# Optimization experiments

Hardware: AMD Instinct MI355X
Metric: run time of the kernel (lower is better)

## Reference

```python
import jax, jax.numpy as jnp
import numpy as np

N = 50000      # nodes
E = 640000     # edges (before self loops)
IN = 128       # in_channels
H = 4          # heads (layer 1)
C = 64         # hidden_channels per head
OUT = 64       # out_channels
SLOPE = 0.2    # PyG GATConv default negative_slope


def setup_inputs() -> dict:
    key = jax.random.key(0)
    ks = jax.random.split(key, 12)
    x = jax.random.normal(ks[0], (N, IN), dtype=jnp.float32)
    edge_src = jax.random.randint(ks[1], (E,), 0, N, dtype=jnp.int32)
    edge_dst = jax.random.randint(ks[2], (E,), 0, N, dtype=jnp.int32)
    # Layer 1 params: Linear IN -> H*C, attention vectors a_src/a_dst [H, C], bias [H*C]
    W1 = jax.random.normal(ks[3], (IN, H * C), dtype=jnp.float32) / np.sqrt(IN)
    att_src1 = jax.random.normal(ks[4], (H, C), dtype=jnp.float32) / np.sqrt(C)
    att_dst1 = jax.random.normal(ks[5], (H, C), dtype=jnp.float32) / np.sqrt(C)
    b1 = jnp.zeros((H * C,), dtype=jnp.float32)
    # Layer 2 params: Linear H*C -> OUT, 1 head
    W2 = jax.random.normal(ks[6], (H * C, OUT), dtype=jnp.float32) / np.sqrt(H * C)
    att_src2 = jax.random.normal(ks[7], (1, OUT), dtype=jnp.float32) / np.sqrt(OUT)
    att_dst2 = jax.random.normal(ks[8], (1, OUT), dtype=jnp.float32) / np.sqrt(OUT)
    b2 = jnp.zeros((OUT,), dtype=jnp.float32)
    return {"x": x, "W1": W1, "att_src1": att_src1, "att_dst1": att_dst1, "b1": b1,
            "W2": W2, "att_src2": att_src2, "att_dst2": att_dst2, "b2": b2,
            "edge_src": edge_src, "edge_dst": edge_dst}


def gat_conv(x, src, dst, W, a_src, a_dst, b, heads, ch):
    """PyG GATConv (concat=True): gather -> LeakyReLU attention -> per-dst softmax -> scatter-add."""
    n = x.shape[0]
    h = (x @ W).reshape(n, heads, ch)                  # [N, H, C]
    al_s = jnp.sum(h * a_src, axis=-1)                 # [N, H] node-level src attention term
    al_d = jnp.sum(h * a_dst, axis=-1)                 # [N, H]
    e = jax.nn.leaky_relu(al_s[src] + al_d[dst], SLOPE)  # [E, H] edge scores
    m = jax.ops.segment_max(e, dst, num_segments=n)    # stable per-dst softmax
    ex = jnp.exp(e - m[dst])
    den = jax.ops.segment_sum(ex, dst, num_segments=n)
    alpha = ex / den[dst]                              # [E, H]
    msg = h[src] * alpha[:, :, None]                   # [E, H, C]
    out = jax.ops.segment_sum(msg, dst, num_segments=n)  # [N, H, C]
    return out.reshape(n, heads * ch) + b


def reference(x, W1, att_src1, att_dst1, b1, W2, att_src2, att_dst2, b2, edge_src, edge_dst):
    # PyG GATConv default add_self_loops=True
    loops = jnp.arange(N, dtype=edge_src.dtype)
    src = jnp.concatenate([edge_src, loops])
    dst = jnp.concatenate([edge_dst, loops])
    h = gat_conv(x, src, dst, W1, att_src1, att_dst1, b1, H, C)
    h = jax.nn.elu(h)                                  # F.elu; dropout p=0 -> no-op
    out = gat_conv(h, src, dst, W2, att_src2, att_dst2, b2, 1, OUT)
    return out
```

## Files before the change

### kernel.cpp

```cpp
#include <hip/hip_runtime.h>
#include <hip/hip_bf16.h>
#include <cstdint>
#include <cstddef>

#define N_NODES 50000
#define N_EDGES 640000
#define ET (N_EDGES + N_NODES)
#define IN_CH 128
#define H1 4
#define HC1 256
#define OUT_CH 64
#define SLOPE 0.2f
#define SCAN_NBLK ((N_NODES + 255) / 256)
#define XW (N_NODES * IN_CH / 8)
#define W1N (IN_CH * HC1)
#define W2N (HC1 * OUT_CH)
#define CONVB ((XW + W1N + W2N + 255) / 256)
#define EDGEB ((ET + 255) / 256)
#define MT ((N_NODES + 63) / 64)
#define G1B (4 * MT)

typedef __attribute__((ext_vector_type(8))) short short8;
typedef __attribute__((ext_vector_type(4))) float floatx4;

__device__ __forceinline__ float bf2f(unsigned short u) {
    return __uint_as_float(((unsigned)u) << 16);
}
__device__ __forceinline__ unsigned short f2bf(float f) {
    unsigned u = __float_as_uint(f);
    unsigned r = 0x7fffu + ((u >> 16) & 1u);
    return (unsigned short)((u + r) >> 16);
}
__device__ __forceinline__ float ldf(const void* p, size_t i, bool f32) {
    return f32 ? ((const float*)p)[i] : bf2f(((const unsigned short*)p)[i]);
}

__global__ __launch_bounds__(256) void init_all(
    const unsigned short* __restrict__ x, unsigned* __restrict__ flag,
    int* __restrict__ counts, int* __restrict__ state)
{
    int b = blockIdx.x;
    if (b < SCAN_NBLK) {
        int i = b * 256 + threadIdx.x;
        if (i < N_NODES) counts[i] = 0;
    } else {
        int t = threadIdx.x;
        if (t < 64) {
            int bad = 0;
            #pragma unroll
            for (int r = 0; r < 4; ++r) {
                float v = bf2f(x[r * 64 + t]);
                if (!(v == v) || fabsf(v) > 1e4f) bad = 1;
            }
            unsigned long long m = __ballot(bad != 0);
            if (t == 0) *flag = (m != 0ull) ? 1u : 0u;
        } else if (t == 64) {
            state[0] = 0; state[1] = 0;
        }
    }
}

__global__ __launch_bounds__(256) void conv_count(
    const void* __restrict__ x, const void* __restrict__ W1,
    const void* __restrict__ W2, const unsigned* __restrict__ flag,
    unsigned short* __restrict__ x16,
    unsigned short* __restrict__ Wt1, unsigned short* __restrict__ Wt2,
    const int* __restrict__ edst, int* __restrict__ counts)
{
    int b = blockIdx.x;
    if (b < CONVB) {
        int i = b * 256 + threadIdx.x;
        const bool f32 = (*flag != 0);
        if (i < XW) {
            size_t off = (size_t)i * 8;
            uint4 st;
            if (f32) {
                const float* xp = (const float*)x + off;
                float4 a = *(const float4*)xp;
                float4 c = *(const float4*)(xp + 4);
                st.x = (unsigned)f2bf(a.x) | ((unsigned)f2bf(a.y) << 16);
                st.y = (unsigned)f2bf(a.z) | ((unsigned)f2bf(a.w) << 16);
                st.z = (unsigned)f2bf(c.x) | ((unsigned)f2bf(c.y) << 16);
                st.w = (unsigned)f2bf(c.z) | ((unsigned)f2bf(c.w) << 16);
            } else {
                st = *(const uint4*)((const unsigned short*)x + off);
            }
            *(uint4*)(x16 + off) = st;
        } else if (i < XW + W1N) {
            int j = i - XW;
            int n = j / IN_CH, k = j % IN_CH;
            Wt1[j] = f2bf(ldf(W1, (size_t)k * HC1 + n, f32));
        } else if (i < XW + W1N + W2N) {
            int j = i - XW - W1N;
            int n = j / HC1, k = j % HC1;
            Wt2[j] = f2bf(ldf(W2, (size_t)k * OUT_CH + n, f32));
        }
    } else {
        int i = (b - CONVB) * 256 + threadIdx.x;
        if (i < ET) {
            int d = (i < N_EDGES) ? edst[i] : (i - N_EDGES);
            atomicAdd(&counts[d], 1);
        }
    }
}

__global__ __launch_bounds__(256) void scan_onepass(
    const int* __restrict__ counts, int* __restrict__ rowptr,
    int* __restrict__ cursor, int* __restrict__ bsum,
    int* __restrict__ boff, int* __restrict__ state)
{
    __shared__ int s[256];
    const int t = threadIdx.x, b = blockIdx.x;
    const int i = b * 256 + t;
    int v = (i < N_NODES) ? counts[i] : 0;
    s[t] = v;
    __syncthreads();
    #pragma unroll
    for (int off = 1; off < 256; off <<= 1) {
        int u = (t >= off) ? s[t - off] : 0;
        __syncthreads();
        s[t] += u;
        __syncthreads();
    }
    const int incl = s[t];
    if (t == 255) {
        __hip_atomic_store(&bsum[b], incl, __ATOMIC_RELAXED, __HIP_MEMORY_SCOPE_AGENT);
        __hip_atomic_fetch_add(&state[0], 1, __ATOMIC_ACQ_REL, __HIP_MEMORY_SCOPE_AGENT);
    }
    if (b == 0) {
        if (t == 0) {
            while (__hip_atomic_load(&state[0], __ATOMIC_ACQUIRE, __HIP_MEMORY_SCOPE_AGENT) < SCAN_NBLK)
                __builtin_amdgcn_s_sleep(8);
        }
        __syncthreads();
        int w = (t < SCAN_NBLK)
              ? __hip_atomic_load(&bsum[t], __ATOMIC_RELAXED, __HIP_MEMORY_SCOPE_AGENT) : 0;
        s[t] = w;
        __syncthreads();
        #pragma unroll
        for (int off = 1; off < 256; off <<= 1) {
            int u = (t >= off) ? s[t - off] : 0;
            __syncthreads();
            s[t] += u;
            __syncthreads();
        }
        if (t < SCAN_NBLK)
            __hip_atomic_store(&boff[t], s[t] - w, __ATOMIC_RELAXED, __HIP_MEMORY_SCOPE_AGENT);
        __syncthreads();
        if (t == 0)
            __hip_atomic_store(&state[1], 1, __ATOMIC_RELEASE, __HIP_MEMORY_SCOPE_AGENT);
    }
    if (t == 0) {
        while (__hip_atomic_load(&state[1], __ATOMIC_ACQUIRE, __HIP_MEMORY_SCOPE_AGENT) == 0)
            __builtin_amdgcn_s_sleep(8);
    }
    __syncthreads();
    int off0 = __hip_atomic_load(&boff[b], __ATOMIC_RELAXED, __HIP_MEMORY_SCOPE_AGENT);
    if (i < N_NODES) {
        int r = off0 + incl - v;
        rowptr[i] = r; cursor[i] = r;
    }
    if (i == 0) rowptr[N_NODES] = ET;
}

template <int KK>
__device__ __forceinline__ void gemm_body(
    const unsigned short* __restrict__ A, const unsigned short* __restrict__ Bt,
    const void* __restrict__ avs, const void* __restrict__ avd,
    const unsigned* __restrict__ flag, unsigned short* __restrict__ C,
    float* __restrict__ als, float* __restrict__ ald,
    int M, int N, int bx, int by)
{
    const int tid = threadIdx.x;
    const int m0 = by * 64, n0 = bx * 64;
    const int w = tid >> 6, lane = tid & 63;
    const int ln = lane & 15, quad = lane >> 4;
    const int m_frag = m0 + w * 16 + ln;
    floatx4 acc[4] = {{0.f,0.f,0.f,0.f},{0.f,0.f,0.f,0.f},{0.f,0.f,0.f,0.f},{0.f,0.f,0.f,0.f}};

    #pragma unroll
    for (int ks = 0; ks < KK / 32; ++ks) {
        const int kbase = ks * 32 + quad * 8;
        short8 a;
        if (m_frag < M) {
            a = *(const short8*)(A + (size_t)m_frag * KK + kbase);
        } else {
            #pragma unroll
            for (int j = 0; j < 8; ++j) a[j] = 0;
        }
        #pragma unroll
        for (int sub = 0; sub < 4; ++sub) {
            short8 b = *(const short8*)(Bt + (size_t)(n0 + sub * 16 + ln) * KK + kbase);
            acc[sub] = __builtin_amdgcn_mfma_f32_16x16x32_bf16(a, b, acc[sub], 0, 0, 0);
        }
    }

    #pragma unroll
    for (int sub = 0; sub < 4; ++sub) {
        #pragma unroll
        for (int r = 0; r < 4; ++r) {
            int m = m0 + w * 16 + quad * 4 + r;
            if (m < M)
                C[(size_t)m * N + n0 + sub * 16 + ln] = f2bf(acc[sub][r]);
        }
    }

    const bool f32in = (*flag != 0);
    float as[4], av[4];
    #pragma unroll
    for (int sub = 0; sub < 4; ++sub) {
        as[sub] = ldf(avs, n0 + sub * 16 + ln, f32in);
        av[sub] = ldf(avd, n0 + sub * 16 + ln, f32in);
    }
    const int Hh = N >> 6;
    #pragma unroll
    for (int r = 0; r < 4; ++r) {
        float ps = 0.f, pd = 0.f;
        #pragma unroll
        for (int sub = 0; sub < 4; ++sub) {
            ps += acc[sub][r] * as[sub];
            pd += acc[sub][r] * av[sub];
        }
        #pragma unroll
        for (int off = 1; off < 16; off <<= 1) {
            ps += __shfl_xor(ps, off, 64);
            pd += __shfl_xor(pd, off, 64);
        }
        int m = m0 + w * 16 + quad * 4 + r;
        if (ln == 0 && m < M) {
            als[(size_t)m * Hh + bx] = ps;
            ald[(size_t)m * Hh + bx] = pd;
        }
    }
}

__global__ __launch_bounds__(256) void gemm1_fill(
    const unsigned short* __restrict__ x16, const unsigned short* __restrict__ Wt1,
    const void* __restrict__ as1, const void* __restrict__ ad1,
    const unsigned* __restrict__ flag, unsigned short* __restrict__ h16,
    float* __restrict__ als, float* __restrict__ ald,
    const int* __restrict__ esrc, const int* __restrict__ edst,
    int* __restrict__ cursor, int* __restrict__ ecsr)
{
    int b = blockIdx.x;
    if (b < G1B) {
        gemm_body<IN_CH>(x16, Wt1, as1, ad1, flag, h16, als, ald,
                         N_NODES, HC1, b & 3, b >> 2);
    } else {
        int i = (b - G1B) * 256 + threadIdx.x;
        if (i < ET) {
            int s = (i < N_EDGES) ? esrc[i] : (i - N_EDGES);
            int d = (i < N_EDGES) ? edst[i] : (i - N_EDGES);
            int pos = atomicAdd(&cursor[d], 1);
            ecsr[pos] = s;
        }
    }
}

__global__ __launch_bounds__(256) void gemm2(
    const unsigned short* __restrict__ xo16, const unsigned short* __restrict__ Wt2,
    const void* __restrict__ as2, const void* __restrict__ ad2,
    const unsigned* __restrict__ flag, unsigned short* __restrict__ h2,
    float* __restrict__ als, float* __restrict__ ald)
{
    gemm_body<HC1>(xo16, Wt2, as2, ad2, flag, h2, als, ald,
                   N_NODES, OUT_CH, 0, blockIdx.x);
}

__global__ __launch_bounds__(256) void agg_node1(
    const int* __restrict__ rowptr, const int* __restrict__ ecsr,
    const unsigned short* __restrict__ h, const float* __restrict__ als,
    const float* __restrict__ ald, const void* __restrict__ bias,
    const unsigned* __restrict__ flag, unsigned short* __restrict__ out)
{
    int wave = (blockIdx.x * blockDim.x + threadIdx.x) >> 6;
    int lane = threadIdx.x & 63;
    if (wave >= N_NODES) return;
    const int d = wave;
    const int hg = lane >> 4;
    const int c0 = (lane & 15) << 2;
    const int lo = rowptr[d], hi = rowptr[d + 1];
    const float ad = ald[d * H1 + hg];

    float acc0 = 0.f, acc1 = 0.f, acc2 = 0.f, acc3 = 0.f, den = 0.f;

    int e = lo;
    for (; e + 3 < hi; e += 4) {
        int s0 = ecsr[e], s1 = ecsr[e + 1], s2 = ecsr[e + 2], s3 = ecsr[e + 3];
        uint2 q0 = *(const uint2*)(h + (size_t)s0 * HC1 + hg * 64 + c0);
        uint2 q1 = *(const uint2*)(h + (size_t)s1 * HC1 + hg * 64 + c0);
        uint2 q2 = *(const uint2*)(h + (size_t)s2 * HC1 + hg * 64 + c0);
        uint2 q3 = *(const uint2*)(h + (size_t)s3 * HC1 + hg * 64 + c0);
        float t0 = als[s0 * H1 + hg] + ad;
        float t1 = als[s1 * H1 + hg] + ad;
        float t2 = als[s2 * H1 + hg] + ad;
        float t3 = als[s3 * H1 + hg] + ad;
        t0 = (t0 > 0.f) ? t0 : SLOPE * t0;
        t1 = (t1 > 0.f) ? t1 : SLOPE * t1;
        t2 = (t2 > 0.f) ? t2 : SLOPE * t2;
        t3 = (t3 > 0.f) ? t3 : SLOPE * t3;
        float p0 = __expf(t0), p1 = __expf(t1), p2 = __expf(t2), p3 = __expf(t3);
        den += (p0 + p1) + (p2 + p3);
        acc0 += p0 * __uint_as_float(q0.x << 16)         + p1 * __uint_as_float(q1.x << 16)
              + p2 * __uint_as_float(q2.x << 16)         + p3 * __uint_as_float(q3.x << 16);
        acc1 += p0 * __uint_as_float(q0.x & 0xffff0000u) + p1 * __uint_as_float(q1.x & 0xffff0000u)
              + p2 * __uint_as_float(q2.x & 0xffff0000u) + p3 * __uint_as_float(q3.x & 0xffff0000u);
        acc2 += p0 * __uint_as_float(q0.y << 16)         + p1 * __uint_as_float(q1.y << 16)
              + p2 * __uint_as_float(q2.y << 16)         + p3 * __uint_as_float(q3.y << 16);
        acc3 += p0 * __uint_as_float(q0.y & 0xffff0000u) + p1 * __uint_as_float(q1.y & 0xffff0000u)
              + p2 * __uint_as_float(q2.y & 0xffff0000u) + p3 * __uint_as_float(q3.y & 0xffff0000u);
    }
    for (; e < hi; ++e) {
        int s0 = ecsr[e];
        uint2 q0 = *(const uint2*)(h + (size_t)s0 * HC1 + hg * 64 + c0);
        float t0 = als[s0 * H1 + hg] + ad;
        t0 = (t0 > 0.f) ? t0 : SLOPE * t0;
        float p0 = __expf(t0);
        den += p0;
        acc0 += p0 * __uint_as_float(q0.x << 16);
        acc1 += p0 * __uint_as_float(q0.x & 0xffff0000u);
        acc2 += p0 * __uint_as_float(q0.y << 16);
        acc3 += p0 * __uint_as_float(q0.y & 0xffff0000u);
    }

    const bool f32in = (*flag != 0);
    const float inv = 1.f / den;
    float v0 = acc0 * inv + ldf(bias, hg * 64 + c0 + 0, f32in);
    float v1 = acc1 * inv + ldf(bias, hg * 64 + c0 + 1, f32in);
    float v2 = acc2 * inv + ldf(bias, hg * 64 + c0 + 2, f32in);
    float v3 = acc3 * inv + ldf(bias, hg * 64 + c0 + 3, f32in);
    v0 = (v0 > 0.f) ? v0 : (__expf(v0) - 1.f);
    v1 = (v1 > 0.f) ? v1 : (__expf(v1) - 1.f);
    v2 = (v2 > 0.f) ? v2 : (__expf(v2) - 1.f);
    v3 = (v3 > 0.f) ? v3 : (__expf(v3) - 1.f);
    uint2 st;
    st.x = (unsigned)f2bf(v0) | ((unsigned)f2bf(v1) << 16);
    st.y = (unsigned)f2bf(v2) | ((unsigned)f2bf(v3) << 16);
    *(uint2*)(out + (size_t)d * HC1 + hg * 64 + c0) = st;
}

__global__ __launch_bounds__(256) void agg_node2(
    const int* __restrict__ rowptr, const int* __restrict__ ecsr,
    const unsigned short* __restrict__ h, const float* __restrict__ als,
    const float* __restrict__ ald, const void* __restrict__ bias,
    const unsigned* __restrict__ flag, float* __restrict__ out)
{
    int wave = (blockIdx.x * blockDim.x + threadIdx.x) >> 6;
    int lane = threadIdx.x & 63;
    if (wave >= N_NODES) return;
    const int d = wave;
    const int eg = lane >> 3;
    const int c0 = (lane & 7) << 3;
    const int lo = rowptr[d], hi = rowptr[d + 1];
    const float ad = ald[d];

    float acc[8];
    #pragma unroll
    for (int j = 0; j < 8; ++j) acc[j] = 0.f;
    float den = 0.f;

    for (int eb = lo; eb < hi; eb += 8) {
        int e = eb + eg;
        if (e < hi) {
            int s = ecsr[e];
            uint4 q = *(const uint4*)(h + (size_t)s * OUT_CH + c0);
            float t = als[s] + ad;
            t = (t > 0.f) ? t : SLOPE * t;
            float p = __expf(t);
            den += p;
            acc[0] += p * __uint_as_float(q.x << 16);
            acc[1] += p * __uint_as_float(q.x & 0xffff0000u);
            acc[2] += p * __uint_as_float(q.y << 16);
            acc[3] += p * __uint_as_float(q.y & 0xffff0000u);
            acc[4] += p * __uint_as_float(q.z << 16);
            acc[5] += p * __uint_as_float(q.z & 0xffff0000u);
            acc[6] += p * __uint_as_float(q.w << 16);
            acc[7] += p * __uint_as_float(q.w & 0xffff0000u);
        }
    }
    #pragma unroll
    for (int off = 8; off <= 32; off <<= 1) {
        den += __shfl_xor(den, off, 64);
        #pragma unroll
        for (int j = 0; j < 8; ++j) acc[j] += __shfl_xor(acc[j], off, 64);
    }
    if (lane < 8) {
        const bool f32in = (*flag != 0);
        const float inv = 1.f / den;
        float4 v0, v1;
        v0.x = acc[0] * inv + ldf(bias, c0 + 0, f32in);
        v0.y = acc[1] * inv + ldf(bias, c0 + 1, f32in);
        v0.z = acc[2] * inv + ldf(bias, c0 + 2, f32in);
        v0.w = acc[3] * inv + ldf(bias, c0 + 3, f32in);
        v1.x = acc[4] * inv + ldf(bias, c0 + 4, f32in);
        v1.y = acc[5] * inv + ldf(bias, c0 + 5, f32in);
        v1.z = acc[6] * inv + ldf(bias, c0 + 6, f32in);
        v1.w = acc[7] * inv + ldf(bias, c0 + 7, f32in);
        *(float4*)(out + (size_t)d * OUT_CH + c0) = v0;
        *(float4*)(out + (size_t)d * OUT_CH + c0 + 4) = v1;
    }
}

extern "C" void kernel_launch(void* const* d_in, const int* in_sizes, int n_in,
                              void* d_out, int out_size, void* d_ws, size_t ws_size,
                              hipStream_t stream)
{
    const void* x   = d_in[0];
    const void* W1  = d_in[1];
    const void* as1 = d_in[2];
    const void* ad1 = d_in[3];
    const void* b1  = d_in[4];
    const void* W2  = d_in[5];
    const void* as2 = d_in[6];
    const void* ad2 = d_in[7];
    const void* b2  = d_in[8];
    const int* esrc = (const int*)d_in[9];
    const int* edst = (const int*)d_in[10];
    float* out = (float*)d_out;

    char* base = (char*)d_ws;
    const size_t MB = 1024 * 1024;
    unsigned short* x16  = (unsigned short*)(base);
    unsigned short* h16  = (unsigned short*)(base + 13 * MB);
    unsigned short* xo16 = (unsigned short*)(base + 39 * MB);
    unsigned short* h2   = (unsigned short*)(base + 65 * MB);
    float* als    = (float*)(base + 72 * MB);
    float* ald    = (float*)(base + 73 * MB);
    unsigned short* Wt1 = (unsigned short*)(base + 74 * MB);
    unsigned short* Wt2 = (unsigned short*)(base + 75 * MB);
    int* counts   = (int*)(base + 76 * MB);
    int* rowptr   = (int*)(base + 77 * MB);
    int* cursor   = (int*)(base + 78 * MB);
    int* ecsr     = (int*)(base + 79 * MB);
    int* bsum     = (int*)(base + 82 * MB);
    int* boff     = bsum + 256;
    int* state    = boff + 256;
    unsigned* flag = (unsigned*)(base + 83 * MB);

    const int BLK = 256;
    const int node_wave_blocks = (N_NODES * 64 + BLK - 1) / BLK;

    init_all<<<SCAN_NBLK + 1, BLK, 0, stream>>>(
        (const unsigned short*)x, flag, counts, state);

    conv_count<<<CONVB + EDGEB, BLK, 0, stream>>>(
        x, W1, W2, flag, x16, Wt1, Wt2, edst, counts);

    scan_onepass<<<SCAN_NBLK, BLK, 0, stream>>>(
        counts, rowptr, cursor, bsum, boff, state);

    gemm1_fill<<<G1B + EDGEB, BLK, 0, stream>>>(
        x16, Wt1, as1, ad1, flag, h16, als, ald, esrc, edst, cursor, ecsr);

    agg_node1<<<node_wave_blocks, BLK, 0, stream>>>(
        rowptr, ecsr, h16, als, ald, b1, flag, xo16);

    gemm2<<<MT, BLK, 0, stream>>>(xo16, Wt2, as2, ad2, flag, h2, als, ald);

    agg_node2<<<node_wave_blocks, BLK, 0, stream>>>(
        rowptr, ecsr, h2, als, ald, b2, flag, out);
}
```

Baseline: 304.1 us.

## Fuse x fp32-to-bf16 conversion into GEMM1 and batch K-loop loads

Removes the separate pass that converts x into a bf16 workspace copy; GEMM1 now reads x directly (fp32 or bf16 per the runtime flag) and converts it in registers. The GEMM inner loop is restructured to issue all A and B fragment loads for a 128-wide K chunk before the MFMAs, to expose more memory-level parallelism. This saves a full write and re-read of the x copy, at the cost of higher register pressure and redundant conversion work, since x rows are re-read by the four column-tile blocks.

```diff
diff --git a/kernel.cpp b/kernel.cpp
--- a/kernel.cpp
+++ b/kernel.cpp
@@ -12,10 +12,9 @@
 #define OUT_CH 64
 #define SLOPE 0.2f
 #define SCAN_NBLK ((N_NODES + 255) / 256)
-#define XW (N_NODES * IN_CH / 8)
 #define W1N (IN_CH * HC1)
 #define W2N (HC1 * OUT_CH)
-#define CONVB ((XW + W1N + W2N + 255) / 256)
+#define CONVB ((W1N + W2N + 255) / 256)
 #define EDGEB ((ET + 255) / 256)
 #define MT ((N_NODES + 63) / 64)
 #define G1B (4 * MT)
@@ -61,9 +60,8 @@
 }
 
 __global__ __launch_bounds__(256) void conv_count(
-    const void* __restrict__ x, const void* __restrict__ W1,
-    const void* __restrict__ W2, const unsigned* __restrict__ flag,
-    unsigned short* __restrict__ x16,
+    const void* __restrict__ W1, const void* __restrict__ W2,
+    const unsigned* __restrict__ flag,
     unsigned short* __restrict__ Wt1, unsigned short* __restrict__ Wt2,
     const int* __restrict__ edst, int* __restrict__ counts)
 {
@@ -71,27 +69,11 @@
     if (b < CONVB) {
         int i = b * 256 + threadIdx.x;
         const bool f32 = (*flag != 0);
-        if (i < XW) {
-            size_t off = (size_t)i * 8;
-            uint4 st;
-            if (f32) {
-                const float* xp = (const float*)x + off;
-                float4 a = *(const float4*)xp;
-                float4 c = *(const float4*)(xp + 4);
-                st.x = (unsigned)f2bf(a.x) | ((unsigned)f2bf(a.y) << 16);
-                st.y = (unsigned)f2bf(a.z) | ((unsigned)f2bf(a.w) << 16);
-                st.z = (unsigned)f2bf(c.x) | ((unsigned)f2bf(c.y) << 16);
-                st.w = (unsigned)f2bf(c.z) | ((unsigned)f2bf(c.w) << 16);
-            } else {
-                st = *(const uint4*)((const unsigned short*)x + off);
-            }
-            *(uint4*)(x16 + off) = st;
-        } else if (i < XW + W1N) {
-            int j = i - XW;
-            int n = j / IN_CH, k = j % IN_CH;
-            Wt1[j] = f2bf(ldf(W1, (size_t)k * HC1 + n, f32));
-        } else if (i < XW + W1N + W2N) {
-            int j = i - XW - W1N;
+        if (i < W1N) {
+            int n = i / IN_CH, k = i % IN_CH;
+            Wt1[i] = f2bf(ldf(W1, (size_t)k * HC1 + n, f32));
+        } else if (i < W1N + W2N) {
+            int j = i - W1N;
             int n = j / HC1, k = j % HC1;
             Wt2[j] = f2bf(ldf(W2, (size_t)k * OUT_CH + n, f32));
         }
@@ -163,9 +145,9 @@
     if (i == 0) rowptr[N_NODES] = ET;
 }
 
-template <int KK>
+template <int KK, bool AWS>
 __device__ __forceinline__ void gemm_body(
-    const unsigned short* __restrict__ A, const unsigned short* __restrict__ Bt,
+    const void* __restrict__ A, const unsigned short* __restrict__ Bt,
     const void* __restrict__ avs, const void* __restrict__ avd,
     const unsigned* __restrict__ flag, unsigned short* __restrict__ C,
     float* __restrict__ als, float* __restrict__ ald,
@@ -176,22 +158,45 @@
     const int w = tid >> 6, lane = tid & 63;
     const int ln = lane & 15, quad = lane >> 4;
     const int m_frag = m0 + w * 16 + ln;
+    const bool af32 = (!AWS) && (*flag != 0);
     floatx4 acc[4] = {{0.f,0.f,0.f,0.f},{0.f,0.f,0.f,0.f},{0.f,0.f,0.f,0.f},{0.f,0.f,0.f,0.f}};
 
     #pragma unroll
-    for (int ks = 0; ks < KK / 32; ++ks) {
-        const int kbase = ks * 32 + quad * 8;
-        short8 a;
-        if (m_frag < M) {
-            a = *(const short8*)(A + (size_t)m_frag * KK + kbase);
-        } else {
+    for (int kc = 0; kc < KK / 128; ++kc) {
+        short8 a[4];
+        short8 b[4][4];
+        #pragma unroll
+        for (int ks = 0; ks < 4; ++ks) {
+            const int kbase = kc * 128 + ks * 32 + quad * 8;
+            if (m_frag < M) {
+                if (af32) {
+                    const float* ap = (const float*)A + (size_t)m_frag * KK + kbase;
+                    float4 f0 = *(const float4*)ap;
+                    float4 f1 = *(const float4*)(ap + 4);
+                    a[ks][0] = (short)f2bf(f0.x); a[ks][1] = (short)f2bf(f0.y);
+                    a[ks][2] = (short)f2bf(f0.z); a[ks][3] = (short)f2bf(f0.w);
+                    a[ks][4] = (short)f2bf(f1.x); a[ks][5] = (short)f2bf(f1.y);
+                    a[ks][6] = (short)f2bf(f1.z); a[ks][7] = (short)f2bf(f1.w);
+                } else {
+                    a[ks] = *(const short8*)((const unsigned short*)A + (size_t)m_frag * KK + kbase);
+                }
+            } else {
+                #pragma unroll
+                for (int j = 0; j < 8; ++j) a[ks][j] = 0;
+            }
+        }
+        #pragma unroll
+        for (int ks = 0; ks < 4; ++ks) {
+            const int kbase = kc * 128 + ks * 32 + quad * 8;
             #pragma unroll
-            for (int j = 0; j < 8; ++j) a[j] = 0;
-        }
-        #pragma unroll
-        for (int sub = 0; sub < 4; ++sub) {
-            short8 b = *(const short8*)(Bt + (size_t)(n0 + sub * 16 + ln) * KK + kbase);
-            acc[sub] = __builtin_amdgcn_mfma_f32_16x16x32_bf16(a, b, acc[sub], 0, 0, 0);
+            for (int sub = 0; sub < 4; ++sub)
+                b[ks][sub] = *(const short8*)(Bt + (size_t)(n0 + sub * 16 + ln) * KK + kbase);
+        }
+        #pragma unroll
+        for (int ks = 0; ks < 4; ++ks) {
+            #pragma unroll
+            for (int sub = 0; sub < 4; ++sub)
+                acc[sub] = __builtin_amdgcn_mfma_f32_16x16x32_bf16(a[ks], b[ks][sub], acc[sub], 0, 0, 0);
         }
     }
 
@@ -235,7 +240,7 @@
 }
 
 __global__ __launch_bounds__(256) void gemm1_fill(
-    const unsigned short* __restrict__ x16, const unsigned short* __restrict__ Wt1,
+    const void* __restrict__ x, const unsigned short* __restrict__ Wt1,
     const void* __restrict__ as1, const void* __restrict__ ad1,
     const unsigned* __restrict__ flag, unsigned short* __restrict__ h16,
     float* __restrict__ als, float* __restrict__ ald,
@@ -244,8 +249,8 @@
 {
     int b = blockIdx.x;
     if (b < G1B) {
-        gemm_body<IN_CH>(x16, Wt1, as1, ad1, flag, h16, als, ald,
-                         N_NODES, HC1, b & 3, b >> 2);
+        gemm_body<IN_CH, false>(x, Wt1, as1, ad1, flag, h16, als, ald,
+                                N_NODES, HC1, b & 3, b >> 2);
     } else {
         int i = (b - G1B) * 256 + threadIdx.x;
         if (i < ET) {
@@ -263,8 +268,8 @@
     const unsigned* __restrict__ flag, unsigned short* __restrict__ h2,
     float* __restrict__ als, float* __restrict__ ald)
 {
-    gemm_body<HC1>(xo16, Wt2, as2, ad2, flag, h2, als, ald,
-                   N_NODES, OUT_CH, 0, blockIdx.x);
+    gemm_body<HC1, true>(xo16, Wt2, as2, ad2, flag, h2, als, ald,
+                         N_NODES, OUT_CH, 0, blockIdx.x);
 }
 
 __global__ __launch_bounds__(256) void agg_node1(
@@ -420,7 +425,6 @@
 
     char* base = (char*)d_ws;
     const size_t MB = 1024 * 1024;
-    unsigned short* x16  = (unsigned short*)(base);
     unsigned short* h16  = (unsigned short*)(base + 13 * MB);
     unsigned short* xo16 = (unsigned short*)(base + 39 * MB);
     unsigned short* h2   = (unsigned short*)(base + 65 * MB);
@@ -444,13 +448,13 @@
         (const unsigned short*)x, flag, counts, state);
 
     conv_count<<<CONVB + EDGEB, BLK, 0, stream>>>(
-        x, W1, W2, flag, x16, Wt1, Wt2, edst, counts);
+        W1, W2, flag, Wt1, Wt2, edst, counts);
 
     scan_onepass<<<SCAN_NBLK, BLK, 0, stream>>>(
         counts, rowptr, cursor, bsum, boff, state);
 
     gemm1_fill<<<G1B + EDGEB, BLK, 0, stream>>>(
-        x16, Wt1, as1, ad1, flag, h16, als, ald, esrc, edst, cursor, ecsr);
+        x, Wt1, as1, ad1, flag, h16, als, ald, esrc, edst, cursor, ecsr);
 
     agg_node1<<<node_wave_blocks, BLK, 0, stream>>>(
         rowptr, ecsr, h16, als, ald, b1, flag, xo16);
```

Result: slower. 327.3 us (+7.7%).
